# Performance work log

Measured on AMD Instinct MI355X. Metric: run time of the kernel, lower is better.

## Reference

```python
import jax, jax.numpy as jnp
import numpy as np

DT = 0.1       # time separation between grid points (forward dt arg default)
UT = 0.1       # stationary-mode time constant
K_IN, K_OUT, K_STATE = 8, 4, 128
PRE_LEN, FWD_LEN, BATCH = 64, 128, 4096


def setup_inputs() -> dict:
    key = jax.random.key(0)
    ks = jax.random.split(key, 16)
    H = K_STATE
    s = 0.05  # small init keeps the 128-step integration numerically tame
    d = {}
    d['pre_x'] = jax.random.normal(ks[0], (PRE_LEN, BATCH, K_IN), jnp.float32)
    d['pre_y'] = jax.random.normal(ks[1], (PRE_LEN, BATCH, K_OUT), jnp.float32)
    d['forward_x'] = jax.random.normal(ks[2], (FWD_LEN, BATCH, K_IN), jnp.float32)
    # encoder nn.GRU (1 layer), torch gate order r,z,n
    d['W_ih'] = jax.random.normal(ks[3], (3 * H, K_IN + K_OUT), jnp.float32) * s
    d['W_hh'] = jax.random.normal(ks[4], (3 * H, H), jnp.float32) * s
    d['b_ih'] = jax.random.normal(ks[5], (3 * H,), jnp.float32) * s
    d['b_hh'] = jax.random.normal(ks[6], (3 * H,), jnp.float32) * s
    # expand_input: Linear(k_in, k_state) + Tanh
    d['W_e'] = jax.random.normal(ks[7], (H, K_IN), jnp.float32) * s
    d['b_e'] = jax.random.normal(ks[8], (H,), jnp.float32) * s
    # ODE GRU cell (BasicCell with net_type='GRU'): input size = k_state
    d['Wc_ih'] = jax.random.normal(ks[9], (3 * H, H), jnp.float32) * s
    d['Wc_hh'] = jax.random.normal(ks[10], (3 * H, H), jnp.float32) * s
    d['bc_ih'] = jax.random.normal(ks[11], (3 * H,), jnp.float32) * s
    d['bc_hh'] = jax.random.normal(ks[12], (3 * H,), jnp.float32) * s
    # fc: Linear(H, 2H, bias=False) -> Tanh -> Linear(2H, k_out, bias=False)
    d['W1'] = jax.random.normal(ks[13], (2 * H, H), jnp.float32) * s
    d['W2'] = jax.random.normal(ks[14], (K_OUT, 2 * H), jnp.float32) * s
    return d


def _gru_cell(x, h, Wi, Wh, bi, bh):
    gi = x @ Wi.T + bi
    gh = h @ Wh.T + bh
    ir, iz, inn = jnp.split(gi, 3, axis=-1)
    hr, hz, hn = jnp.split(gh, 3, axis=-1)
    r = jax.nn.sigmoid(ir + hr)
    z = jax.nn.sigmoid(iz + hz)
    n = jnp.tanh(inn + r * hn)
    return (1.0 - z) * n + z * h


def reference(pre_x, pre_y, forward_x, W_ih, W_hh, b_ih, b_hh, W_e, b_e,
              Wc_ih, Wc_hh, bc_ih, bc_hh, W1, W2):
    H = W_hh.shape[1]
    # ---- GRU encoder over [pre_x, pre_y], take final hidden state ----
    enc_in = jnp.concatenate([pre_x, pre_y], axis=2)  # [Tp, B, k_in+k_out]
    h0 = jnp.zeros((enc_in.shape[1], H), enc_in.dtype)

    def enc_step(h, x):
        return _gru_cell(x, h, W_ih, W_hh, b_ih, b_hh), None

    hn, _ = jax.lax.scan(enc_step, h0, enc_in)  # [B, H]

    # ---- natural cubic spline of the control input over the grid ----
    L = forward_x.shape[0]
    hs = DT
    ys = jnp.concatenate([pre_x[-1:], forward_x], axis=0)  # [L+1, B, k_in]
    rhs = 6.0 * (ys[:-2] - 2.0 * ys[1:-1] + ys[2:]) / (hs * hs)  # [L-1, ...]
    nin = L - 1
    A = 4.0 * jnp.eye(nin) + jnp.eye(nin, k=1) + jnp.eye(nin, k=-1)
    Minner = jnp.linalg.solve(A, rhs.reshape(nin, -1)).reshape(rhs.shape)
    zpad = jnp.zeros_like(ys[:1])
    M = jnp.concatenate([zpad, Minner, zpad], axis=0)  # 2nd derivs, [L+1,B,k_in]

    def u(t):
        i = jnp.clip(jnp.floor(t / hs).astype(jnp.int32), 0, L - 1)
        t0 = i.astype(ys.dtype) * hs
        a = (t0 + hs - t) / hs
        b = (t - t0) / hs
        yi, yi1 = jnp.take(ys, i, axis=0), jnp.take(ys, i + 1, axis=0)
        Mi, Mi1 = jnp.take(M, i, axis=0), jnp.take(M, i + 1, axis=0)
        return a * yi + b * yi1 + ((a ** 3 - a) * Mi + (b ** 3 - b) * Mi1) * (hs * hs) / 6.0

    # ---- ODE system: stationary GRU-cell dynamics ----
    def f(t, y):
        x = jnp.tanh(u(t) @ W_e.T + b_e)
        return (_gru_cell(x, y, Wc_ih, Wc_hh, bc_ih, bc_hh) - y) / UT

    # ---- fixed-grid RK4 (torchdiffeq method='rk4', one step per interval) ----
    def rk4(y, t0):
        k1 = f(t0, y)
        k2 = f(t0 + hs / 2, y + (hs / 2) * k1)
        k3 = f(t0 + hs / 2, y + (hs / 2) * k2)
        k4 = f(t0 + hs, y + hs * k3)
        yn = y + (hs / 6.0) * (k1 + 2 * k2 + 2 * k3 + k4)
        return yn, yn

    t_starts = jnp.arange(L, dtype=ys.dtype) * hs
    _, traj = jax.lax.scan(rk4, hn, t_starts)  # [L, B, H]

    # ---- output head: Linear -> Tanh -> Linear (no bias) ----
    return jnp.tanh(traj @ W1.T) @ W2.T  # [L, B, k_out]
```

## Files before the change

### kernel.cpp

```cpp
#include <hip/hip_runtime.h>
#include <math.h>

#define NB    4096
#define NH    128
#define NKIN  8
#define NKOUT 4
#define NTP   64
#define NL    128
#define BKIN  (NB*NKIN)
#define LOG2E 1.44269504088896340736f

typedef __attribute__((ext_vector_type(8))) short short8;
typedef __attribute__((ext_vector_type(4))) float f32x4;

#if __has_builtin(__builtin_amdgcn_exp2f)
#define EXP2F __builtin_amdgcn_exp2f
#else
#define EXP2F exp2f
#endif

__device__ __forceinline__ short f2bf(float f) {
    union { float f; unsigned u; } v; v.f = f;
    unsigned u = v.u;
    return (short)((u + 0x7fffu + ((u >> 16) & 1u)) >> 16);
}
__device__ __forceinline__ unsigned pkbf2(float a, float b) {
#if __has_builtin(__builtin_amdgcn_cvt_pk_bf16_f32)
    auto p = __builtin_amdgcn_cvt_pk_bf16_f32(a, b);
    unsigned q; __builtin_memcpy(&q, &p, 4); return q;
#else
    union { float f; unsigned u; } x, y; x.f = a; y.f = b;
    unsigned ua = (x.u + 0x7fffu + ((x.u >> 16) & 1u)) >> 16;
    unsigned ub = (y.u + 0x7fffu + ((y.u >> 16) & 1u)) & 0xffff0000u;
    return ua | ub;
#endif
}
__device__ __forceinline__ void st4(short* dst, const f32x4& v) {
    uint2 q; q.x = pkbf2(v[0], v[1]); q.y = pkbf2(v[2], v[3]);
    *(uint2*)dst = q;
}

__global__ void spline_um_kernel(const float* __restrict__ pre_x,
                                 const float* __restrict__ fx,
                                 float* __restrict__ UM)
{
    __shared__ float cp[128];
    if (threadIdx.x == 0) {
        float c = 0.f;
        for (int j = 1; j <= 127; ++j) { c = 1.0f/(4.0f - c); cp[j] = c; }
    }
    __syncthreads();
    int col = blockIdx.x*128 + threadIdx.x;
    const float r6 = 6.0f/(0.1f*0.1f);
    const float KK = 0.01f/16.0f;
    float y0 = pre_x[(size_t)(NTP-1)*BKIN + col];
    float y1 = fx[col];
    float d = 0.f;
    for (int j = 1; j <= 127; ++j) {
        float y2 = fx[(size_t)j*BKIN + col];
        float r  = r6*(y0 - 2.f*y1 + y2);
        d = (r - d)*cp[j];
        UM[(size_t)j*BKIN + col] = d;
        y0 = y1; y1 = y2;
    }
    float xn  = 0.f;
    float yj1 = fx[(size_t)127*BKIN + col];
    for (int j = 127; j >= 1; --j) {
        float dj = UM[(size_t)j*BKIN + col];
        float x  = dj - cp[j]*xn;
        float yj = fx[(size_t)(j-1)*BKIN + col];
        UM[(size_t)j*BKIN + col] = 0.5f*(yj + yj1) - KK*(x + xn);
        xn = x; yj1 = yj;
    }
    float ys0 = pre_x[(size_t)(NTP-1)*BKIN + col];
    UM[col] = 0.5f*(ys0 + yj1) - KK*xn;
}

__global__ void prep_frags(const float* __restrict__ W1, const float* __restrict__ W2,
                           short* __restrict__ w1f, short* __restrict__ w2f)
{
    int tid = threadIdx.x;
    for (int idx = tid; idx < 16*4*64*8; idx += 256) {
        int j = idx & 7, lane = (idx >> 3) & 63, kc = (idx >> 9) & 3, t = idx >> 11;
        int row = t*16 + (lane & 15);
        int k   = kc*32 + (lane >> 4)*8 + j;
        w1f[idx] = f2bf(2.0f*LOG2E*W1[row*NH + k]);
    }
    for (int idx = tid; idx < 8*64*8; idx += 256) {
        int j = idx & 7, lane = (idx >> 3) & 63, kc = idx >> 9;
        int m = lane & 15;
        int k = kc*32 + (lane >> 4)*8 + j;
        w2f[idx] = (m < NKOUT) ? f2bf(W2[m*2*NH + k]) : (short)0;
    }
}

__device__ __forceinline__ void gemmB(const short* bp, const short8 (&A)[3][4], f32x4 (&acc)[3])
{
    #pragma unroll
    for (int kc = 0; kc < 4; ++kc) {
        short8 b = *(const short8*)(bp + kc*32);
        #pragma unroll
        for (int g = 0; g < 3; ++g)
            acc[g] = __builtin_amdgcn_mfma_f32_16x16x32_bf16(A[g][kc], b, acc[g], 0, 0, 0);
    }
}

__device__ __forceinline__ void gateK(const f32x4 (&gi)[3], const f32x4 (&gh)[3],
                                      const f32x4& yin, f32x4& K)
{
    #pragma unroll
    for (int r = 0; r < 4; ++r) {
        float rg = __builtin_amdgcn_rcpf(1.0f + EXP2F(gi[0][r] + gh[0][r]));
        float zg = __builtin_amdgcn_rcpf(1.0f + EXP2F(gi[1][r] + gh[1][r]));
        float tg = 1.0f - 2.0f*__builtin_amdgcn_rcpf(1.0f + EXP2F(gi[2][r] + rg*gh[2][r]));
        K[r] = (1.0f - zg)*(tg - yin[r]);
    }
}

__global__ void __launch_bounds__(512, 2)
fused_kernel(const float* __restrict__ pre_x, const float* __restrict__ pre_y,
             const float* __restrict__ fx,
             const float* __restrict__ W_ih, const float* __restrict__ W_hh,
             const float* __restrict__ b_ih, const float* __restrict__ b_hh,
             const float* __restrict__ W_e,  const float* __restrict__ b_e,
             const float* __restrict__ Wc_ih,const float* __restrict__ Wc_hh,
             const float* __restrict__ bc_ih,const float* __restrict__ bc_hh,
             const float* __restrict__ UM,   const short* __restrict__ w1f,
             const short* __restrict__ w2f,  float* __restrict__ out)
{
    __shared__ __align__(16) short yT [16*136];
    __shared__ __align__(16) short E0 [16*136];
    __shared__ __align__(16) short E1 [16*136];
    __shared__ __align__(16) short xmT[16*136];
    __shared__ __align__(16) short x1T[16*136];
    __shared__ __align__(16) short UMb[16*40];
    __shared__ __align__(16) short U1b[16*40];
    __shared__ __align__(16) short oT [16*264];

    const int tid  = threadIdx.x;
    const int w    = tid >> 6;
    const int lane = tid & 63;
    const int quad = lane >> 4;
    const int m    = lane & 15;
    const int hq   = w*16 + quad*4;
    const int b0   = blockIdx.x * 16;
    const f32x4 z4 = {0.f, 0.f, 0.f, 0.f};

    for (int i = tid; i < 16*136; i += 512) yT[i] = 0;
    for (int i = tid; i < 16*40;  i += 512) { UMb[i] = 0; U1b[i] = 0; }

    const float scg[3] = {-LOG2E, -LOG2E, 2.0f*LOG2E};

    short8 Ahh[3][4], Aih[3][4];
    #pragma unroll
    for (int g = 0; g < 3; ++g)
        #pragma unroll
        for (int c = 0; c < 4; ++c) {
            const float* ph = Wc_hh + (size_t)(g*NH + w*16 + m)*NH + c*32 + quad*8;
            const float* pi = Wc_ih + (size_t)(g*NH + w*16 + m)*NH + c*32 + quad*8;
            short8 fh, fi;
            #pragma unroll
            for (int j = 0; j < 8; ++j) { fh[j] = f2bf(scg[g]*ph[j]); fi[j] = f2bf(scg[g]*pi[j]); }
            Ahh[g][c] = fh; Aih[g][c] = fi;
        }
    short8 Aexp;
    #pragma unroll
    for (int j = 0; j < 8; ++j) {
        int k = quad*8 + j;
        Aexp[j] = (k < NKIN) ? f2bf(2.0f*LOG2E*W_e[(w*16 + m)*NKIN + k]) : (short)0;
    }
    f32x4 brz4, bzz4, bgn4, bin4, be4;
    #pragma unroll
    for (int r = 0; r < 4; ++r) {
        int h = hq + r;
        brz4[r] = -LOG2E*(bc_ih[h]      + bc_hh[h]);
        bzz4[r] = -LOG2E*(bc_ih[NH + h] + bc_hh[NH + h]);
        bgn4[r] = 2.0f*LOG2E*bc_hh[2*NH + h];
        bin4[r] = 2.0f*LOG2E*bc_ih[2*NH + h];
        be4[r]  = 2.0f*LOG2E*b_e[h];
    }

    f32x4 y = z4;

    {
        short8 Ehh[3][4];
        #pragma unroll
        for (int g = 0; g < 3; ++g)
            #pragma unroll
            for (int c = 0; c < 4; ++c) {
                const float* ph = W_hh + (size_t)(g*NH + w*16 + m)*NH + c*32 + quad*8;
                short8 fh;
                #pragma unroll
                for (int j = 0; j < 8; ++j) fh[j] = f2bf(scg[g]*ph[j]);
                Ehh[g][c] = fh;
            }
        short8 Eih[3];
        #pragma unroll
        for (int g = 0; g < 3; ++g) {
            short8 f1;
            #pragma unroll
            for (int j = 0; j < 8; ++j) {
                int k = quad*8 + j;
                f1[j] = (k < 12) ? f2bf(scg[g]*W_ih[(size_t)(g*NH + w*16 + m)*12 + k]) : (short)0;
            }
            Eih[g] = f1;
        }
        f32x4 erz4, ezz4, egn4, ein4;
        #pragma unroll
        for (int r = 0; r < 4; ++r) {
            int h = hq + r;
            erz4[r] = -LOG2E*(b_ih[h]      + b_hh[h]);
            ezz4[r] = -LOG2E*(b_ih[NH + h] + b_hh[NH + h]);
            egn4[r] = 2.0f*LOG2E*b_hh[2*NH + h];
            ein4[r] = 2.0f*LOG2E*b_ih[2*NH + h];
        }
        const int eb = tid / 12, ek = tid - eb*12;
        float encv = 0.f;
        if (tid < 192)
            encv = (ek < NKIN) ? pre_x[((size_t)0*NB + b0 + eb)*NKIN + ek]
                               : pre_y[((size_t)0*NB + b0 + eb)*NKOUT + (ek - NKIN)];
        __syncthreads();
        for (int t = 0; t < NTP; ++t) {
            if (tid < 192) {
                UMb[eb*40 + ek] = f2bf(encv);
                if (t + 1 < NTP)
                    encv = (ek < NKIN) ? pre_x[((size_t)(t+1)*NB + b0 + eb)*NKIN + ek]
                                       : pre_y[((size_t)(t+1)*NB + b0 + eb)*NKOUT + (ek - NKIN)];
            }
            __syncthreads();
            f32x4 gi[3] = {z4, z4, ein4};
            {
                short8 b = *(const short8*)(UMb + m*40 + quad*8);
                #pragma unroll
                for (int g = 0; g < 3; ++g)
                    gi[g] = __builtin_amdgcn_mfma_f32_16x16x32_bf16(Eih[g], b, gi[g], 0, 0, 0);
            }
            f32x4 gh[3] = {erz4, ezz4, egn4};
            gemmB(yT + m*136 + quad*8, Ehh, gh);
            f32x4 K;
            gateK(gi, gh, y, K);
            #pragma unroll
            for (int r = 0; r < 4; ++r) y[r] += K[r];
            __syncthreads();
            st4(yT + m*136 + hq, y);
        }
    }

    if (tid < 64) UMb[(tid >> 2)*40 + 8 + (tid & 3)] = 0;
    const int sb = tid >> 3, sk = tid & 7;
    const size_t scol = (size_t)(b0 + sb)*NKIN + sk;
    if (tid < 128) UMb[sb*40 + sk] = f2bf(pre_x[(size_t)(NTP-1)*BKIN + scol]);
    __syncthreads();
    {
        short8 b = *(const short8*)(UMb + m*40 + quad*8);
        f32x4 c0 = be4;
        c0 = __builtin_amdgcn_mfma_f32_16x16x32_bf16(Aexp, b, c0, 0, 0, 0);
        f32x4 xv;
        #pragma unroll
        for (int r = 0; r < 4; ++r)
            xv[r] = 1.0f - 2.0f*__builtin_amdgcn_rcpf(1.0f + EXP2F(c0[r]));
        st4(xmT + m*136 + hq, xv);
    }
    __syncthreads();
    f32x4 gi0[3] = {z4, z4, bin4};
    gemmB(xmT + m*136 + quad*8, Aih, gi0);
    if (tid < 128) { UMb[sb*40 + sk] = f2bf(UM[scol]); U1b[sb*40 + sk] = f2bf(fx[scol]); }
    __syncthreads();
    {
        short8 bm = *(const short8*)(UMb + m*40 + quad*8);
        short8 b1 = *(const short8*)(U1b + m*40 + quad*8);
        f32x4 cm = be4, c1 = be4;
        cm = __builtin_amdgcn_mfma_f32_16x16x32_bf16(Aexp, bm, cm, 0, 0, 0);
        c1 = __builtin_amdgcn_mfma_f32_16x16x32_bf16(Aexp, b1, c1, 0, 0, 0);
        f32x4 xm, x1;
        #pragma unroll
        for (int r = 0; r < 4; ++r) {
            xm[r] = 1.0f - 2.0f*__builtin_amdgcn_rcpf(1.0f + EXP2F(cm[r]));
            x1[r] = 1.0f - 2.0f*__builtin_amdgcn_rcpf(1.0f + EXP2F(c1[r]));
        }
        st4(xmT + m*136 + hq, xm);
        st4(x1T + m*136 + hq, x1);
    }
    __syncthreads();
    f32x4 gim[3] = {z4, z4, bin4}, gi1[3] = {z4, z4, bin4};
    gemmB(xmT + m*136 + quad*8, Aih, gim);
    gemmB(x1T + m*136 + quad*8, Aih, gi1);
    float fxv = 0.f, umv = 0.f;
    if (tid < 128) { fxv = fx[BKIN + scol]; umv = UM[BKIN + scol]; }

    for (int st = 0; st < NL; ++st) {
        f32x4 gh[3] = {brz4, bzz4, bgn4};
        gemmB(yT + m*136 + quad*8, Ahh, gh);
        f32x4 K, Ks, ye;
        gateK(gi0, gh, y, K);
        #pragma unroll
        for (int r = 0; r < 4; ++r) { Ks[r] = K[r]; ye[r] = y[r] + 0.5f*K[r]; }
        st4(E0 + m*136 + hq, ye);
        __syncthreads();
        gh[0] = brz4; gh[1] = bzz4; gh[2] = bgn4;
        gemmB(E0 + m*136 + quad*8, Ahh, gh);
        gateK(gim, gh, ye, K);
        #pragma unroll
        for (int r = 0; r < 4; ++r) { Ks[r] += 2.f*K[r]; ye[r] = y[r] + 0.5f*K[r]; }
        st4(E1 + m*136 + hq, ye);
        __syncthreads();
        gh[0] = brz4; gh[1] = bzz4; gh[2] = bgn4;
        gemmB(E1 + m*136 + quad*8, Ahh, gh);
        gateK(gim, gh, ye, K);
        #pragma unroll
        for (int r = 0; r < 4; ++r) { Ks[r] += 2.f*K[r]; ye[r] = y[r] + K[r]; }
        st4(E0 + m*136 + hq, ye);
        __syncthreads();
        gh[0] = brz4; gh[1] = bzz4; gh[2] = bgn4;
        gemmB(E0 + m*136 + quad*8, Ahh, gh);
        gateK(gi1, gh, ye, K);
        #pragma unroll
        for (int r = 0; r < 4; ++r) y[r] += (1.0f/6.0f)*(Ks[r] + K[r]);
        st4(yT + m*136 + hq, y);
        if (tid < 128) { UMb[sb*40 + sk] = f2bf(umv); U1b[sb*40 + sk] = f2bf(fxv); }
        short8 a1f[2][4];
        #pragma unroll
        for (int kc = 0; kc < 4; ++kc) {
            a1f[0][kc] = *(const short8*)(w1f + (size_t)((w*4      + kc)*64 + lane)*8);
            a1f[1][kc] = *(const short8*)(w1f + (size_t)(((w+8)*4 + kc)*64 + lane)*8);
        }
        __syncthreads();
        {
            short8 bm = *(const short8*)(UMb + m*40 + quad*8);
            short8 b1 = *(const short8*)(U1b + m*40 + quad*8);
            f32x4 cm = be4, c1 = be4;
            cm = __builtin_amdgcn_mfma_f32_16x16x32_bf16(Aexp, bm, cm, 0, 0, 0);
            c1 = __builtin_amdgcn_mfma_f32_16x16x32_bf16(Aexp, b1, c1, 0, 0, 0);
            f32x4 xm, x1;
            #pragma unroll
            for (int r = 0; r < 4; ++r) {
                xm[r] = 1.0f - 2.0f*__builtin_amdgcn_rcpf(1.0f + EXP2F(cm[r]));
                x1[r] = 1.0f - 2.0f*__builtin_amdgcn_rcpf(1.0f + EXP2F(c1[r]));
            }
            st4(xmT + m*136 + hq, xm);
            st4(x1T + m*136 + hq, x1);
        }
        {
            f32x4 o0 = z4, o1 = z4;
            #pragma unroll
            for (int kc = 0; kc < 4; ++kc) {
                short8 b = *(const short8*)(yT + m*136 + quad*8 + kc*32);
                o0 = __builtin_amdgcn_mfma_f32_16x16x32_bf16(a1f[0][kc], b, o0, 0, 0, 0);
                o1 = __builtin_amdgcn_mfma_f32_16x16x32_bf16(a1f[1][kc], b, o1, 0, 0, 0);
            }
            f32x4 t0, t1;
            #pragma unroll
            for (int r = 0; r < 4; ++r) {
                t0[r] = 1.0f - 2.0f*__builtin_amdgcn_rcpf(1.0f + EXP2F(o0[r]));
                t1[r] = 1.0f - 2.0f*__builtin_amdgcn_rcpf(1.0f + EXP2F(o1[r]));
            }
            st4(oT + m*264 + w*16     + quad*4, t0);
            st4(oT + m*264 + (w+8)*16 + quad*4, t1);
        }
        if (tid < 128) {
            if (st + 2 < NL) { fxv = fx[(size_t)(st+2)*BKIN + scol]; umv = UM[(size_t)(st+2)*BKIN + scol]; }
            else             { fxv = 0.f; umv = 0.f; }
        }
        short8 a2f[8];
        if (w == (st & 7)) {
            #pragma unroll
            for (int kc = 0; kc < 8; ++kc)
                a2f[kc] = *(const short8*)(w2f + (size_t)(kc*64 + lane)*8);
        }
        __syncthreads();
        if (w == (st & 7)) {
            f32x4 oc = z4;
            #pragma unroll
            for (int kc = 0; kc < 8; ++kc) {
                short8 b = *(const short8*)(oT + m*264 + kc*32 + quad*8);
                oc = __builtin_amdgcn_mfma_f32_16x16x32_bf16(a2f[kc], b, oc, 0, 0, 0);
            }
            if (quad == 0)
                *(f32x4*)(out + ((size_t)st*NB + b0 + m)*NKOUT) = oc;
        }
        gi0[0] = gi1[0]; gi0[1] = gi1[1]; gi0[2] = gi1[2];
        gim[0] = z4; gim[1] = z4; gim[2] = bin4;
        gi1[0] = z4; gi1[1] = z4; gi1[2] = bin4;
        gemmB(xmT + m*136 + quad*8, Aih, gim);
        gemmB(x1T + m*136 + quad*8, Aih, gi1);
    }
}

extern "C" void kernel_launch(void* const* d_in, const int* in_sizes, int n_in,
                              void* d_out, int out_size, void* d_ws, size_t ws_size,
                              hipStream_t stream)
{
    const float* pre_x = (const float*)d_in[0];
    const float* pre_y = (const float*)d_in[1];
    const float* fx    = (const float*)d_in[2];
    const float* W_ih  = (const float*)d_in[3];
    const float* W_hh  = (const float*)d_in[4];
    const float* b_ih  = (const float*)d_in[5];
    const float* b_hh  = (const float*)d_in[6];
    const float* W_e   = (const float*)d_in[7];
    const float* b_e   = (const float*)d_in[8];
    const float* Wc_ih = (const float*)d_in[9];
    const float* Wc_hh = (const float*)d_in[10];
    const float* bc_ih = (const float*)d_in[11];
    const float* bc_hh = (const float*)d_in[12];
    const float* W1    = (const float*)d_in[13];
    const float* W2    = (const float*)d_in[14];
    float* out = (float*)d_out;

    float* UM  = (float*)d_ws;
    short* w1f = (short*)((char*)d_ws + (size_t)NL*NB*NKIN*4);
    short* w2f = w1f + 16*4*64*8;

    prep_frags<<<dim3(1), dim3(256), 0, stream>>>(W1, W2, w1f, w2f);
    spline_um_kernel<<<dim3((NB*NKIN)/128), dim3(128), 0, stream>>>(pre_x, fx, UM);
    fused_kernel<<<dim3(NB/16), dim3(512), 0, stream>>>(
        pre_x, pre_y, fx, W_ih, W_hh, b_ih, b_hh, W_e, b_e,
        Wc_ih, Wc_hh, bc_ih, bc_hh, UM, w1f, w2f, out);
}
```

Before: 798.3 us.

## Double-buffer GRU state in LDS and defer output head to cut barriers

The encoder loop now ping-pongs both the hidden-state and input buffers, which takes it from two barriers per step to one and prefetches inputs two steps ahead. In the RK4 loop the output head for step st-1 is computed inside step st, overlapping the previous barrier phases, and the W1 fragments are hoisted into registers once. This drops one barrier per RK4 step, at the cost of more live registers and an epilogue for the last step.

```diff
diff --git a/kernel.cpp b/kernel.cpp
--- a/kernel.cpp
+++ b/kernel.cpp
@@ -38,6 +38,9 @@
 __device__ __forceinline__ void st4(short* dst, const f32x4& v) {
     uint2 q; q.x = pkbf2(v[0], v[1]); q.y = pkbf2(v[2], v[3]);
     *(uint2*)dst = q;
+}
+__device__ __forceinline__ float tanh2(float a2) {
+    return 1.0f - 2.0f*__builtin_amdgcn_rcpf(1.0f + EXP2F(a2));
 }
 
 __global__ void spline_um_kernel(const float* __restrict__ pre_x,
@@ -104,7 +107,6 @@
             acc[g] = __builtin_amdgcn_mfma_f32_16x16x32_bf16(A[g][kc], b, acc[g], 0, 0, 0);
     }
 }
-
 __device__ __forceinline__ void gateK(const f32x4 (&gi)[3], const f32x4 (&gh)[3],
                                       const f32x4& yin, f32x4& K)
 {
@@ -112,7 +114,7 @@
     for (int r = 0; r < 4; ++r) {
         float rg = __builtin_amdgcn_rcpf(1.0f + EXP2F(gi[0][r] + gh[0][r]));
         float zg = __builtin_amdgcn_rcpf(1.0f + EXP2F(gi[1][r] + gh[1][r]));
-        float tg = 1.0f - 2.0f*__builtin_amdgcn_rcpf(1.0f + EXP2F(gi[2][r] + rg*gh[2][r]));
+        float tg = tanh2(gi[2][r] + rg*gh[2][r]);
         K[r] = (1.0f - zg)*(tg - yin[r]);
     }
 }
@@ -128,8 +130,8 @@
              const float* __restrict__ UM,   const short* __restrict__ w1f,
              const short* __restrict__ w2f,  float* __restrict__ out)
 {
-    __shared__ __align__(16) short yT [16*136];
-    __shared__ __align__(16) short E0 [16*136];
+    __shared__ __align__(16) short yTa[16*136];
+    __shared__ __align__(16) short yTb[16*136];
     __shared__ __align__(16) short E1 [16*136];
     __shared__ __align__(16) short xmT[16*136];
     __shared__ __align__(16) short x1T[16*136];
@@ -145,11 +147,84 @@
     const int hq   = w*16 + quad*4;
     const int b0   = blockIdx.x * 16;
     const f32x4 z4 = {0.f, 0.f, 0.f, 0.f};
-
-    for (int i = tid; i < 16*136; i += 512) yT[i] = 0;
+    const float scg[3] = {-LOG2E, -LOG2E, 2.0f*LOG2E};
+
+    for (int i = tid; i < 16*136; i += 512) yTa[i] = 0;
     for (int i = tid; i < 16*40;  i += 512) { UMb[i] = 0; U1b[i] = 0; }
 
-    const float scg[3] = {-LOG2E, -LOG2E, 2.0f*LOG2E};
+    f32x4 y = z4;
+
+    {
+        short8 Ehh[3][4];
+        #pragma unroll
+        for (int g = 0; g < 3; ++g)
+            #pragma unroll
+            for (int c = 0; c < 4; ++c) {
+                const float* ph = W_hh + (size_t)(g*NH + w*16 + m)*NH + c*32 + quad*8;
+                short8 fh;
+                #pragma unroll
+                for (int j = 0; j < 8; ++j) fh[j] = f2bf(scg[g]*ph[j]);
+                Ehh[g][c] = fh;
+            }
+        short8 Eih[3];
+        #pragma unroll
+        for (int g = 0; g < 3; ++g) {
+            short8 f1;
+            #pragma unroll
+            for (int j = 0; j < 8; ++j) {
+                int k = quad*8 + j;
+                f1[j] = (k < 12) ? f2bf(scg[g]*W_ih[(size_t)(g*NH + w*16 + m)*12 + k]) : (short)0;
+            }
+            Eih[g] = f1;
+        }
+        f32x4 erz4, ezz4, egn4, ein4;
+        #pragma unroll
+        for (int r = 0; r < 4; ++r) {
+            int h = hq + r;
+            erz4[r] = -LOG2E*(b_ih[h]      + b_hh[h]);
+            ezz4[r] = -LOG2E*(b_ih[NH + h] + b_hh[NH + h]);
+            egn4[r] = 2.0f*LOG2E*b_hh[2*NH + h];
+            ein4[r] = 2.0f*LOG2E*b_ih[2*NH + h];
+        }
+        const int eb = tid / 12, ek = tid - eb*12;
+        float encv = 0.f;
+        if (tid < 192) {
+            float e0 = (ek < NKIN) ? pre_x[((size_t)0*NB + b0 + eb)*NKIN + ek]
+                                   : pre_y[((size_t)0*NB + b0 + eb)*NKOUT + (ek - NKIN)];
+            UMb[eb*40 + ek] = f2bf(e0);
+            encv = (ek < NKIN) ? pre_x[((size_t)1*NB + b0 + eb)*NKIN + ek]
+                               : pre_y[((size_t)1*NB + b0 + eb)*NKOUT + (ek - NKIN)];
+        }
+        __syncthreads();
+        for (int t = 0; t < NTP; ++t) {
+            float evn = 0.f;
+            if (tid < 192) {
+                int tn = (t + 2 < NTP) ? t + 2 : NTP - 1;
+                evn = (ek < NKIN) ? pre_x[((size_t)tn*NB + b0 + eb)*NKIN + ek]
+                                  : pre_y[((size_t)tn*NB + b0 + eb)*NKOUT + (ek - NKIN)];
+            }
+            const short* bin_buf  = (t & 1) ? U1b : UMb;
+            short*       bout_buf = (t & 1) ? UMb : U1b;
+            const short* sin_buf  = (t & 1) ? yTb : yTa;
+            short*       sout_buf = (t & 1) ? yTa : yTb;
+            f32x4 gi[3] = {z4, z4, ein4};
+            {
+                short8 b = *(const short8*)(bin_buf + m*40 + quad*8);
+                #pragma unroll
+                for (int g = 0; g < 3; ++g)
+                    gi[g] = __builtin_amdgcn_mfma_f32_16x16x32_bf16(Eih[g], b, gi[g], 0, 0, 0);
+            }
+            f32x4 gh[3] = {erz4, ezz4, egn4};
+            gemmB(sin_buf + m*136 + quad*8, Ehh, gh);
+            f32x4 K;
+            gateK(gi, gh, y, K);
+            #pragma unroll
+            for (int r = 0; r < 4; ++r) y[r] += K[r];
+            st4(sout_buf + m*136 + hq, y);
+            if (tid < 192) { bout_buf[eb*40 + ek] = f2bf(encv); encv = evn; }
+            __syncthreads();
+        }
+    }
 
     short8 Ahh[3][4], Aih[3][4];
     #pragma unroll
@@ -168,6 +243,12 @@
     for (int j = 0; j < 8; ++j) {
         int k = quad*8 + j;
         Aexp[j] = (k < NKIN) ? f2bf(2.0f*LOG2E*W_e[(w*16 + m)*NKIN + k]) : (short)0;
+    }
+    short8 A1f[2][4];
+    #pragma unroll
+    for (int kc = 0; kc < 4; ++kc) {
+        A1f[0][kc] = *(const short8*)(w1f + (size_t)(((w    )*4 + kc)*64 + lane)*8);
+        A1f[1][kc] = *(const short8*)(w1f + (size_t)(((w + 8)*4 + kc)*64 + lane)*8);
     }
     f32x4 brz4, bzz4, bgn4, bin4, be4;
     #pragma unroll
@@ -180,75 +261,13 @@
         be4[r]  = 2.0f*LOG2E*b_e[h];
     }
 
-    f32x4 y = z4;
-
-    {
-        short8 Ehh[3][4];
-        #pragma unroll
-        for (int g = 0; g < 3; ++g)
-            #pragma unroll
-            for (int c = 0; c < 4; ++c) {
-                const float* ph = W_hh + (size_t)(g*NH + w*16 + m)*NH + c*32 + quad*8;
-                short8 fh;
-                #pragma unroll
-                for (int j = 0; j < 8; ++j) fh[j] = f2bf(scg[g]*ph[j]);
-                Ehh[g][c] = fh;
-            }
-        short8 Eih[3];
-        #pragma unroll
-        for (int g = 0; g < 3; ++g) {
-            short8 f1;
-            #pragma unroll
-            for (int j = 0; j < 8; ++j) {
-                int k = quad*8 + j;
-                f1[j] = (k < 12) ? f2bf(scg[g]*W_ih[(size_t)(g*NH + w*16 + m)*12 + k]) : (short)0;
-            }
-            Eih[g] = f1;
-        }
-        f32x4 erz4, ezz4, egn4, ein4;
-        #pragma unroll
-        for (int r = 0; r < 4; ++r) {
-            int h = hq + r;
-            erz4[r] = -LOG2E*(b_ih[h]      + b_hh[h]);
-            ezz4[r] = -LOG2E*(b_ih[NH + h] + b_hh[NH + h]);
-            egn4[r] = 2.0f*LOG2E*b_hh[2*NH + h];
-            ein4[r] = 2.0f*LOG2E*b_ih[2*NH + h];
-        }
-        const int eb = tid / 12, ek = tid - eb*12;
-        float encv = 0.f;
-        if (tid < 192)
-            encv = (ek < NKIN) ? pre_x[((size_t)0*NB + b0 + eb)*NKIN + ek]
-                               : pre_y[((size_t)0*NB + b0 + eb)*NKOUT + (ek - NKIN)];
-        __syncthreads();
-        for (int t = 0; t < NTP; ++t) {
-            if (tid < 192) {
-                UMb[eb*40 + ek] = f2bf(encv);
-                if (t + 1 < NTP)
-                    encv = (ek < NKIN) ? pre_x[((size_t)(t+1)*NB + b0 + eb)*NKIN + ek]
-                                       : pre_y[((size_t)(t+1)*NB + b0 + eb)*NKOUT + (ek - NKIN)];
-            }
-            __syncthreads();
-            f32x4 gi[3] = {z4, z4, ein4};
-            {
-                short8 b = *(const short8*)(UMb + m*40 + quad*8);
-                #pragma unroll
-                for (int g = 0; g < 3; ++g)
-                    gi[g] = __builtin_amdgcn_mfma_f32_16x16x32_bf16(Eih[g], b, gi[g], 0, 0, 0);
-            }
-            f32x4 gh[3] = {erz4, ezz4, egn4};
-            gemmB(yT + m*136 + quad*8, Ehh, gh);
-            f32x4 K;
-            gateK(gi, gh, y, K);
-            #pragma unroll
-            for (int r = 0; r < 4; ++r) y[r] += K[r];
-            __syncthreads();
-            st4(yT + m*136 + hq, y);
-        }
-    }
-
-    if (tid < 64) UMb[(tid >> 2)*40 + 8 + (tid & 3)] = 0;
     const int sb = tid >> 3, sk = tid & 7;
     const size_t scol = (size_t)(b0 + sb)*NKIN + sk;
+    if (tid < 128) {
+        short* bb = (tid & 64) ? U1b : UMb;
+        int rr = (tid >> 2) & 15, cc = 8 + (tid & 3);
+        bb[rr*40 + cc] = 0;
+    }
     if (tid < 128) UMb[sb*40 + sk] = f2bf(pre_x[(size_t)(NTP-1)*BKIN + scol]);
     __syncthreads();
     {
@@ -257,8 +276,7 @@
         c0 = __builtin_amdgcn_mfma_f32_16x16x32_bf16(Aexp, b, c0, 0, 0, 0);
         f32x4 xv;
         #pragma unroll
-        for (int r = 0; r < 4; ++r)
-            xv[r] = 1.0f - 2.0f*__builtin_amdgcn_rcpf(1.0f + EXP2F(c0[r]));
+        for (int r = 0; r < 4; ++r) xv[r] = tanh2(c0[r]);
         st4(xmT + m*136 + hq, xv);
     }
     __syncthreads();
@@ -274,10 +292,7 @@
         c1 = __builtin_amdgcn_mfma_f32_16x16x32_bf16(Aexp, b1, c1, 0, 0, 0);
         f32x4 xm, x1;
         #pragma unroll
-        for (int r = 0; r < 4; ++r) {
-            xm[r] = 1.0f - 2.0f*__builtin_amdgcn_rcpf(1.0f + EXP2F(cm[r]));
-            x1[r] = 1.0f - 2.0f*__builtin_amdgcn_rcpf(1.0f + EXP2F(c1[r]));
-        }
+        for (int r = 0; r < 4; ++r) { xm[r] = tanh2(cm[r]); x1[r] = tanh2(c1[r]); }
         st4(xmT + m*136 + hq, xm);
         st4(x1T + m*136 + hq, x1);
     }
@@ -286,45 +301,62 @@
     gemmB(xmT + m*136 + quad*8, Aih, gim);
     gemmB(x1T + m*136 + quad*8, Aih, gi1);
     float fxv = 0.f, umv = 0.f;
-    if (tid < 128) { fxv = fx[BKIN + scol]; umv = UM[BKIN + scol]; }
+    if (tid < 128) { fxv = fx[(size_t)BKIN + scol]; umv = UM[(size_t)BKIN + scol]; }
 
     for (int st = 0; st < NL; ++st) {
         f32x4 gh[3] = {brz4, bzz4, bgn4};
-        gemmB(yT + m*136 + quad*8, Ahh, gh);
+        gemmB(yTa + m*136 + quad*8, Ahh, gh);
+        if (st > 0) {
+            f32x4 o0 = z4, o1 = z4;
+            #pragma unroll
+            for (int kc = 0; kc < 4; ++kc) {
+                short8 b = *(const short8*)(yTa + m*136 + quad*8 + kc*32);
+                o0 = __builtin_amdgcn_mfma_f32_16x16x32_bf16(A1f[0][kc], b, o0, 0, 0, 0);
+                o1 = __builtin_amdgcn_mfma_f32_16x16x32_bf16(A1f[1][kc], b, o1, 0, 0, 0);
+            }
+            f32x4 t0, t1;
+            #pragma unroll
+            for (int r = 0; r < 4; ++r) { t0[r] = tanh2(o0[r]); t1[r] = tanh2(o1[r]); }
+            st4(oT + m*264 + w*16     + quad*4, t0);
+            st4(oT + m*264 + (w+8)*16 + quad*4, t1);
+        }
         f32x4 K, Ks, ye;
         gateK(gi0, gh, y, K);
         #pragma unroll
         for (int r = 0; r < 4; ++r) { Ks[r] = K[r]; ye[r] = y[r] + 0.5f*K[r]; }
-        st4(E0 + m*136 + hq, ye);
-        __syncthreads();
+        st4(yTb + m*136 + hq, ye);
+        __syncthreads();
+        float fxn = 0.f, umn = 0.f;
+        if (tid < 128) {
+            int sn = (st + 2 < NL) ? st + 2 : NL - 1;
+            fxn = fx[(size_t)sn*BKIN + scol];
+            umn = UM[(size_t)sn*BKIN + scol];
+        }
+        if (st > 0 && w == ((st-1) & 7)) {
+            short8 a2f[8];
+            #pragma unroll
+            for (int kc = 0; kc < 8; ++kc)
+                a2f[kc] = *(const short8*)(w2f + (size_t)(kc*64 + lane)*8);
+            f32x4 oc = z4;
+            #pragma unroll
+            for (int kc = 0; kc < 8; ++kc) {
+                short8 b = *(const short8*)(oT + m*264 + kc*32 + quad*8);
+                oc = __builtin_amdgcn_mfma_f32_16x16x32_bf16(a2f[kc], b, oc, 0, 0, 0);
+            }
+            if (quad == 0)
+                *(f32x4*)(out + ((size_t)(st-1)*NB + b0 + m)*NKOUT) = oc;
+        }
+        if (tid < 128) { UMb[sb*40 + sk] = f2bf(umv); U1b[sb*40 + sk] = f2bf(fxv); }
         gh[0] = brz4; gh[1] = bzz4; gh[2] = bgn4;
-        gemmB(E0 + m*136 + quad*8, Ahh, gh);
+        gemmB(yTb + m*136 + quad*8, Ahh, gh);
         gateK(gim, gh, ye, K);
         #pragma unroll
         for (int r = 0; r < 4; ++r) { Ks[r] += 2.f*K[r]; ye[r] = y[r] + 0.5f*K[r]; }
         st4(E1 + m*136 + hq, ye);
+        fxv = fxn; umv = umn;
         __syncthreads();
         gh[0] = brz4; gh[1] = bzz4; gh[2] = bgn4;
         gemmB(E1 + m*136 + quad*8, Ahh, gh);
-        gateK(gim, gh, ye, K);
-        #pragma unroll
-        for (int r = 0; r < 4; ++r) { Ks[r] += 2.f*K[r]; ye[r] = y[r] + K[r]; }
-        st4(E0 + m*136 + hq, ye);
-        __syncthreads();
-        gh[0] = brz4; gh[1] = bzz4; gh[2] = bgn4;
-        gemmB(E0 + m*136 + quad*8, Ahh, gh);
-        gateK(gi1, gh, ye, K);
-        #pragma unroll
-        for (int r = 0; r < 4; ++r) y[r] += (1.0f/6.0f)*(Ks[r] + K[r]);
-        st4(yT + m*136 + hq, y);
-        if (tid < 128) { UMb[sb*40 + sk] = f2bf(umv); U1b[sb*40 + sk] = f2bf(fxv); }
-        short8 a1f[2][4];
-        #pragma unroll
-        for (int kc = 0; kc < 4; ++kc) {
-            a1f[0][kc] = *(const short8*)(w1f + (size_t)((w*4      + kc)*64 + lane)*8);
-            a1f[1][kc] = *(const short8*)(w1f + (size_t)(((w+8)*4 + kc)*64 + lane)*8);
-        }
-        __syncthreads();
         {
             short8 bm = *(const short8*)(UMb + m*40 + quad*8);
             short8 b1 = *(const short8*)(U1b + m*40 + quad*8);
@@ -333,56 +365,59 @@
             c1 = __builtin_amdgcn_mfma_f32_16x16x32_bf16(Aexp, b1, c1, 0, 0, 0);
             f32x4 xm, x1;
             #pragma unroll
-            for (int r = 0; r < 4; ++r) {
-                xm[r] = 1.0f - 2.0f*__builtin_amdgcn_rcpf(1.0f + EXP2F(cm[r]));
-                x1[r] = 1.0f - 2.0f*__builtin_amdgcn_rcpf(1.0f + EXP2F(c1[r]));
-            }
+            for (int r = 0; r < 4; ++r) { xm[r] = tanh2(cm[r]); x1[r] = tanh2(c1[r]); }
             st4(xmT + m*136 + hq, xm);
             st4(x1T + m*136 + hq, x1);
         }
-        {
-            f32x4 o0 = z4, o1 = z4;
-            #pragma unroll
-            for (int kc = 0; kc < 4; ++kc) {
-                short8 b = *(const short8*)(yT + m*136 + quad*8 + kc*32);
-                o0 = __builtin_amdgcn_mfma_f32_16x16x32_bf16(a1f[0][kc], b, o0, 0, 0, 0);
-                o1 = __builtin_amdgcn_mfma_f32_16x16x32_bf16(a1f[1][kc], b, o1, 0, 0, 0);
-            }
-            f32x4 t0, t1;
-            #pragma unroll
-            for (int r = 0; r < 4; ++r) {
-                t0[r] = 1.0f - 2.0f*__builtin_amdgcn_rcpf(1.0f + EXP2F(o0[r]));
-                t1[r] = 1.0f - 2.0f*__builtin_amdgcn_rcpf(1.0f + EXP2F(o1[r]));
-            }
-            st4(oT + m*264 + w*16     + quad*4, t0);
-            st4(oT + m*264 + (w+8)*16 + quad*4, t1);
-        }
-        if (tid < 128) {
-            if (st + 2 < NL) { fxv = fx[(size_t)(st+2)*BKIN + scol]; umv = UM[(size_t)(st+2)*BKIN + scol]; }
-            else             { fxv = 0.f; umv = 0.f; }
-        }
-        short8 a2f[8];
-        if (w == (st & 7)) {
-            #pragma unroll
-            for (int kc = 0; kc < 8; ++kc)
-                a2f[kc] = *(const short8*)(w2f + (size_t)(kc*64 + lane)*8);
-        }
-        __syncthreads();
-        if (w == (st & 7)) {
-            f32x4 oc = z4;
-            #pragma unroll
-            for (int kc = 0; kc < 8; ++kc) {
-                short8 b = *(const short8*)(oT + m*264 + kc*32 + quad*8);
-                oc = __builtin_amdgcn_mfma_f32_16x16x32_bf16(a2f[kc], b, oc, 0, 0, 0);
-            }
-            if (quad == 0)
-                *(f32x4*)(out + ((size_t)st*NB + b0 + m)*NKOUT) = oc;
-        }
+        gateK(gim, gh, ye, K);
+        #pragma unroll
+        for (int r = 0; r < 4; ++r) { Ks[r] += 2.f*K[r]; ye[r] = y[r] + K[r]; }
+        st4(yTb + m*136 + hq, ye);
+        __syncthreads();
+        gh[0] = brz4; gh[1] = bzz4; gh[2] = bgn4;
+        gemmB(yTb + m*136 + quad*8, Ahh, gh);
+        gateK(gi1, gh, ye, K);
+        #pragma unroll
+        for (int r = 0; r < 4; ++r) y[r] += (1.0f/6.0f)*(Ks[r] + K[r]);
+        st4(yTa + m*136 + hq, y);
         gi0[0] = gi1[0]; gi0[1] = gi1[1]; gi0[2] = gi1[2];
         gim[0] = z4; gim[1] = z4; gim[2] = bin4;
         gi1[0] = z4; gi1[1] = z4; gi1[2] = bin4;
         gemmB(xmT + m*136 + quad*8, Aih, gim);
         gemmB(x1T + m*136 + quad*8, Aih, gi1);
+        __syncthreads();
+    }
+
+    {
+        f32x4 o0 = z4, o1 = z4;
+        #pragma unroll
+        for (int kc = 0; kc < 4; ++kc) {
+            short8 b = *(const short8*)(yTa + m*136 + quad*8 + kc*32);
+            o0 = __builtin_amdgcn_mfma_f32_16x16x32_bf16(A1f[0][kc], b, o0, 0, 0, 0);
+            o1 = __builtin_amdgcn_mfma_f32_16x16x32_bf16(A1f[1][kc], b, o1, 0, 0, 0);
+        }
+        f32x4 t0, t1;
+        #pragma unroll
+        for (int r = 0; r < 4; ++r) { t0[r] = tanh2(o0[r]); t1[r] = tanh2(o1[r]); }
+        st4(oT + m*264 + w*16     + quad*4, t0);
+        st4(oT + m*264 + (w+8)*16 + quad*4, t1);
+        short8 a2f[8];
+        if (w == 7) {
+            #pragma unroll
+            for (int kc = 0; kc < 8; ++kc)
+                a2f[kc] = *(const short8*)(w2f + (size_t)(kc*64 + lane)*8);
+        }
+        __syncthreads();
+        if (w == 7) {
+            f32x4 oc = z4;
+            #pragma unroll
+            for (int kc = 0; kc < 8; ++kc) {
+                short8 b = *(const short8*)(oT + m*264 + kc*32 + quad*8);
+                oc = __builtin_amdgcn_mfma_f32_16x16x32_bf16(a2f[kc], b, oc, 0, 0, 0);
+            }
+            if (quad == 0)
+                *(f32x4*)(out + ((size_t)(NL-1)*NB + b0 + m)*NKOUT) = oc;
+        }
     }
 }
 
```

Result: slower. 843.2 us (+5.6%).
